# Kernel tuning notes

Measured on AMD Instinct MI355X. Metric: run time of the kernel, lower is better.

Reference implementation:

```python
import jax, jax.numpy as jnp
import numpy as np

# GATConv hyperparams hardcoded in InterGraphAttention: out_channels=32, heads=2
H = 2
C = 32
N_H = 50000
N_T = 50000
E = 1600000
D = 128
NEG_SLOPE = 0.2


def setup_inputs() -> dict:
    key = jax.random.key(0)
    ks = jax.random.split(key, 9)
    h_x = jax.random.normal(ks[0], (N_H, D), dtype=jnp.float32)
    t_x = jax.random.normal(ks[1], (N_T, D), dtype=jnp.float32)
    src = jax.random.randint(ks[2], (E,), 0, N_H)
    dst = jax.random.randint(ks[3], (E,), 0, N_T)
    # PyG's add_self_loops path first removes existing self-loops; generate edges without any
    dst = jnp.where(dst == src, (dst + 1) % N_T, dst)
    edge_index = jnp.stack([src, dst]).astype(jnp.int64)
    glorot = 1.0 / np.sqrt(D)
    W_src = jax.random.normal(ks[4], (D, H * C), dtype=jnp.float32) * glorot
    W_dst = jax.random.normal(ks[5], (D, H * C), dtype=jnp.float32) * glorot
    att_src = jax.random.normal(ks[6], (H, C), dtype=jnp.float32) * (1.0 / np.sqrt(C))
    att_dst = jax.random.normal(ks[7], (H, C), dtype=jnp.float32) * (1.0 / np.sqrt(C))
    bias = jnp.zeros((H * C,), dtype=jnp.float32)
    return {"h_x": h_x, "t_x": t_x, "edge_index": edge_index,
            "W_src": W_src, "W_dst": W_dst,
            "att_src": att_src, "att_dst": att_dst, "bias": bias}


def _gat(x_src, x_dst, src, dst, W_s, W_d, a_src, a_dst, bias):
    Ns, Nd = x_src.shape[0], x_dst.shape[0]
    xs = (x_src @ W_s).reshape(Ns, H, C)   # [Ns,H,C]
    xd = (x_dst @ W_d).reshape(Nd, H, C)   # [Nd,H,C]
    al_s = jnp.einsum('nhc,hc->nh', xs, a_src)  # [Ns,H]
    al_d = jnp.einsum('nhc,hc->nh', xd, a_dst)  # [Nd,H]
    # PyG GATConv default add_self_loops=True: append i->i for i < min(Ns,Nd)
    loop = jnp.arange(min(Ns, Nd), dtype=src.dtype)
    src2 = jnp.concatenate([src, loop])
    dst2 = jnp.concatenate([dst, loop])
    alpha = jax.nn.leaky_relu(al_s[src2] + al_d[dst2], NEG_SLOPE)  # [E2,H]
    # edge-softmax over destination neighborhoods (PyG softmax: +1e-16 in denom)
    m = jax.ops.segment_max(alpha, dst2, num_segments=Nd)
    e = jnp.exp(alpha - m[dst2])
    s = jax.ops.segment_sum(e, dst2, num_segments=Nd)
    w = e / (s[dst2] + 1e-16)                                      # [E2,H]
    msg = w[:, :, None] * xs[src2]                                 # [E2,H,C]
    out = jax.ops.segment_sum(msg, dst2, num_segments=Nd)          # [Nd,H,C]
    return out.reshape(Nd, H * C) + bias


def reference(h_x, t_x, edge_index, W_src, W_dst, att_src, att_dst, bias):
    h_in = jax.nn.elu(h_x)
    t_in = jax.nn.elu(t_x)
    src, dst = edge_index[0], edge_index[1]
    t_rep = _gat(h_in, t_in, src, dst, W_src, W_dst, att_src, att_dst, bias)
    h_rep = _gat(t_in, h_in, dst, src, W_src, W_dst, att_src, att_dst, bias)
    return (h_rep, t_rep)
```

## Files before the change

kernel.cpp:

```cpp
#include <hip/hip_runtime.h>
#include <hip/hip_bf16.h>
#include <math.h>

#define HC 64
#define DD 128
#define BSH 7
#define BW  128
#define KMAX 512
#define CHUNK 4096
#define CAP 8192
#define CAPB 6144

typedef __attribute__((ext_vector_type(8))) short bf16x8;
typedef __attribute__((ext_vector_type(4))) float f32x4;

__device__ __forceinline__ unsigned short f2bf(float f) {
  unsigned u = __float_as_uint(f);
  return (unsigned short)((u + 0x7fffu + ((u >> 16) & 1u)) >> 16);
}

__global__ __launch_bounds__(128) void build_bt(
    const float* __restrict__ Wsrc, const float* __restrict__ Wdst,
    const float* __restrict__ att_src, const float* __restrict__ att_dst,
    unsigned short* __restrict__ Bt)
{
  int j = blockIdx.x;
  int k = threadIdx.x;
  const float LOG2E = 1.44269504f;
  float v = 0.f;
  if (j < 64) {
    v = Wsrc[k * HC + j];
  } else if (j < 68) {
    int hh = j - 64;
    const float* W = (hh < 2) ? Wsrc : Wdst;
    const float* a = (hh < 2) ? att_src : att_dst;
    int h = hh & 1;
    float s = 0.f;
    for (int c = 0; c < 32; ++c)
      s = fmaf(W[k * HC + h * 32 + c], a[h * 32 + c], s);
    v = s * LOG2E;
  }
  Bt[j * DD + k] = f2bf(v);
}

__global__ __launch_bounds__(256) void node_mfma(
    const float* __restrict__ xH, const float* __restrict__ xT,
    const unsigned short* __restrict__ Bt,
    __hip_bfloat16* __restrict__ xsH, __hip_bfloat16* __restrict__ xsT,
    float* __restrict__ lsH, float* __restrict__ ldH,
    float* __restrict__ lsT, float* __restrict__ ldT,
    int NH, int NT, int blocksH)
{
  const float* x; __hip_bfloat16* xs; float* logit_s; float* logit_d; int N, blk;
  if ((int)blockIdx.x < blocksH) { x = xH; xs = xsH; logit_s = lsH; logit_d = ldH; N = NH; blk = blockIdx.x; }
  else { x = xT; xs = xsT; logit_s = lsT; logit_d = ldT; N = NT; blk = blockIdx.x - blocksH; }

  int tid  = threadIdx.x;
  int wid  = tid >> 6;
  int lane = tid & 63;
  int m    = lane & 15;
  int kg   = lane >> 4;
  int nbase = (blk * 4 + wid) * 16;
  if (nbase >= N) return;
  int nrow = nbase + m;
  int nclamp = (nrow < N) ? nrow : (N - 1);

  bf16x8 ahi[4], alo[4];
  const float* xrow = x + (size_t)nclamp * DD + kg * 8;
  #pragma unroll
  for (int kt = 0; kt < 4; ++kt) {
    float4 v0 = *(const float4*)(xrow + kt * 32);
    float4 v1 = *(const float4*)(xrow + kt * 32 + 4);
    float vv[8] = {v0.x, v0.y, v0.z, v0.w, v1.x, v1.y, v1.z, v1.w};
    #pragma unroll
    for (int i = 0; i < 8; ++i) {
      float v = vv[i];
      v = (v > 0.f) ? v : (exp2f(v * 1.44269504f) - 1.f);
      unsigned hb = __float_as_uint(v) & 0xffff0000u;
      ahi[kt][i] = (short)(hb >> 16);
      alo[kt][i] = (short)f2bf(v - __uint_as_float(hb));
    }
  }

  f32x4 acc[5];
  #pragma unroll
  for (int ct = 0; ct < 5; ++ct) acc[ct] = (f32x4){0.f, 0.f, 0.f, 0.f};
  const unsigned short* bbase = Bt + m * DD + kg * 8;
  #pragma unroll
  for (int ct = 0; ct < 5; ++ct) {
    #pragma unroll
    for (int kt = 0; kt < 4; ++kt) {
      bf16x8 b = *(const bf16x8*)(bbase + ct * 16 * DD + kt * 32);
      acc[ct] = __builtin_amdgcn_mfma_f32_16x16x32_bf16(ahi[kt], b, acc[ct], 0, 0, 0);
      acc[ct] = __builtin_amdgcn_mfma_f32_16x16x32_bf16(alo[kt], b, acc[ct], 0, 0, 0);
    }
  }

  int r0 = kg * 4;
  unsigned short* xsu = (unsigned short*)xs;
  #pragma unroll
  for (int ct = 0; ct < 4; ++ct) {
    #pragma unroll
    for (int r = 0; r < 4; ++r) {
      int n = nbase + r0 + r;
      if (n < N) xsu[(size_t)n * HC + ct * 16 + m] = f2bf(acc[ct][r]);
    }
  }
  if (m < 4) {
    float* dst = (m < 2) ? logit_s : logit_d;
    int h = m & 1;
    #pragma unroll
    for (int r = 0; r < 4; ++r) {
      int n = nbase + r0 + r;
      if (n < N) dst[n * 2 + h] = acc[4][r];
    }
  }
}

__global__ __launch_bounds__(256) void partition_atomic(
    const int* __restrict__ src, const int* __restrict__ dst, int E, int NL,
    int* __restrict__ gcurA, int* __restrict__ gcurB,
    unsigned int* __restrict__ partA, unsigned int* __restrict__ partB,
    int KA, int KB)
{
  __shared__ unsigned int stage[CHUNK];
  __shared__ int lcnt[KMAX];
  __shared__ int lbase[KMAX];
  __shared__ int lcur[KMAX];
  __shared__ int gbase[KMAX];
  int tid = threadIdx.x, bid = blockIdx.x;
  int pass = blockIdx.y;
  const int K = pass ? KB : KA;
  int* gcur = pass ? gcurB : gcurA;
  unsigned int* out = pass ? partB : partA;

  int base = bid * CHUNK;
  int E2 = E + NL;
  int lim = base + CHUNK < E2 ? base + CHUNK : E2;
  int cnt = lim - base;

  for (int i = tid; i < K; i += 256) lcnt[i] = 0;
  __syncthreads();
  for (int i = base + tid; i < lim; i += 256) {
    int s, d;
    if (i < E) { s = src[i]; d = dst[i]; } else { s = d = i - E; }
    int key = pass ? s : d;
    atomicAdd(&lcnt[key >> BSH], 1);
  }
  __syncthreads();
  if (tid < 64) {
    int carry = 0;
    for (int c0 = 0; c0 < K; c0 += 64) {
      int c = c0 + tid;
      int v = (c < K) ? lcnt[c] : 0;
      int inc = v;
      #pragma unroll
      for (int o = 1; o < 64; o <<= 1) {
        int u = __shfl_up(inc, o, 64);
        if (tid >= o) inc += u;
      }
      if (c < K) lbase[c] = inc - v + carry;
      carry += __shfl(inc, 63, 64);
    }
  }
  __syncthreads();
  for (int k = tid; k < K; k += 256) {
    lcur[k] = lbase[k];
    gbase[k] = atomicAdd(&gcur[k], lcnt[k]);
  }
  __syncthreads();
  for (int i = base + tid; i < lim; i += 256) {
    int s, d;
    if (i < E) { s = src[i]; d = dst[i]; } else { s = d = i - E; }
    int key = pass ? s : d;
    int val = pass ? d : s;
    int pos = atomicAdd(&lcur[key >> BSH], 1);
    stage[pos] = (unsigned int)val | ((unsigned int)key << 16);
  }
  __syncthreads();
  for (int i = tid; i < cnt; i += 256) {
    unsigned int wv = stage[i];
    int k = wv >> (16 + BSH);
    out[(size_t)k * CAPB + gbase[k] + (i - lbase[k])] = wv;
  }
}

__global__ __launch_bounds__(1024) void scan_offsets(
    const int* __restrict__ gcurA, const int* __restrict__ gcurB,
    int KA, int KB, int E2,
    int* __restrict__ offA, int* __restrict__ offB)
{
  __shared__ int buf[1024];
  int t = threadIdx.x;
  int v = (t < KA) ? gcurA[t] : 0;
  buf[t] = v; __syncthreads();
  #pragma unroll
  for (int off = 1; off < 1024; off <<= 1) {
    int u = (t >= off) ? buf[t - off] : 0;
    __syncthreads(); buf[t] += u; __syncthreads();
  }
  if (t < KA) offA[t] = buf[t] - v;
  if (t == 0) offA[KA] = E2;
  __syncthreads();
  int v2 = (t < KB) ? gcurB[t] : 0;
  buf[t] = v2; __syncthreads();
  #pragma unroll
  for (int off = 1; off < 1024; off <<= 1) {
    int u = (t >= off) ? buf[t - off] : 0;
    __syncthreads(); buf[t] += u; __syncthreads();
  }
  if (t < KB) offB[t] = buf[t] - v2;
  if (t == 0) offB[KB] = E2;
}

__global__ __launch_bounds__(256) void bucket_csr3(
    const unsigned int* __restrict__ partA, const int* __restrict__ cntA,
    const int* __restrict__ offA, int KA, int NA,
    const unsigned int* __restrict__ partB, const int* __restrict__ cntB,
    const int* __restrict__ offB, int KB, int NB,
    int E2, int* __restrict__ csrA, int* __restrict__ rowA,
    int* __restrict__ csrB, int* __restrict__ rowB)
{
  __shared__ int sbuf[CAP];
  __shared__ int hist[BW + 1];
  __shared__ int cur[BW];
  const unsigned int* part; const int* off; const int* cntp;
  int* csr; int* row; int k, K, N;
  if ((int)blockIdx.x < KA) { k = blockIdx.x; part = partA; off = offA; cntp = cntA; csr = csrA; row = rowA; K = KA; N = NA; }
  else { k = blockIdx.x - KA; part = partB; off = offB; cntp = cntB; csr = csrB; row = rowB; K = KB; N = NB; }
  int tid = threadIdx.x;
  int beg = off[k];
  int cnt = cntp[k];
  size_t kbase = (size_t)k * CAPB;
  int d0 = k << BSH;
  int width = (BW < N - d0) ? BW : (N - d0);

  for (int i = tid; i <= BW; i += 256) hist[i] = 0;
  __syncthreads();
  for (int i = tid; i < cnt; i += 256)
    atomicAdd(&hist[(part[kbase + i] >> 16) & (BW - 1)], 1);
  __syncthreads();
  if (tid == 0) {
    int run = 0;
    for (int j = 0; j < width; ++j) { int c = hist[j]; hist[j] = run; run += c; }
    hist[width] = run;
  }
  __syncthreads();
  if (tid < width) { cur[tid] = hist[tid]; row[d0 + tid] = beg + hist[tid]; }
  if (k == K - 1 && tid == 0) row[N] = E2;
  __syncthreads();
  if (cnt <= CAP) {
    for (int i = tid; i < cnt; i += 256) {
      unsigned int wv = part[kbase + i];
      int pos = atomicAdd(&cur[(wv >> 16) & (BW - 1)], 1);
      sbuf[pos] = wv & 0xFFFF;
    }
    __syncthreads();
    for (int i = tid; i < cnt; i += 256) csr[beg + i] = sbuf[i];
  } else {
    for (int i = tid; i < cnt; i += 256) {
      unsigned int wv = part[kbase + i];
      int pos = atomicAdd(&cur[(wv >> 16) & (BW - 1)], 1);
      csr[beg + pos] = wv & 0xFFFF;
    }
  }
}

__device__ __forceinline__ float lrelu_clamp(float a) {
  a = (a > 0.f) ? a : 0.2f * a;
  return fminf(a, 43.f);
}

__global__ __launch_bounds__(256) void csr_message5(
    const int* __restrict__ rowA, const int* __restrict__ csrA,
    const float* __restrict__ lsA, const float* __restrict__ ldA,
    const __hip_bfloat16* __restrict__ xsA, float* __restrict__ outA, int NdA,
    const int* __restrict__ rowB, const int* __restrict__ csrB,
    const float* __restrict__ lsB, const float* __restrict__ ldB,
    const __hip_bfloat16* __restrict__ xsB, float* __restrict__ outB, int NdB,
    const float* __restrict__ bias, int blocksA)
{
  const int* row; const int* csr_src; const float* logit_s; const float* logit_d;
  const __hip_bfloat16* xs; float* out; int Nd, blk;
  if ((int)blockIdx.x < blocksA) { row = rowA; csr_src = csrA; logit_s = lsA; logit_d = ldA; xs = xsA; out = outA; Nd = NdA; blk = blockIdx.x; }
  else { row = rowB; csr_src = csrB; logit_s = lsB; logit_d = ldB; xs = xsB; out = outB; Nd = NdB; blk = blockIdx.x - blocksA; }

  __shared__ int lds[4 * 232];
  int tid  = threadIdx.x;
  int wid  = tid >> 6;
  int lane = tid & 63;
  int l31  = lane & 31;
  int half = lane >> 5;
  int head = l31 >> 4;

  int* L = &lds[wid * 232];
  float* Lf = (float*)L;
  int sv_w = (half ? 40 : 0) + l31;
  int w0_w = (half ? 160 : 80) + l31;
  int w1_w = (half ? 200 : 120) + l31;
  const int4*   svq = (const int4*)  (L  + (half ? 40 : 0));
  const float4* wq  = (const float4*)(Lf + (half ? (head ? 200 : 160)
                                                 : (head ? 120 : 80)));
  const unsigned* xs2 = (const unsigned*)xs;
  const float2* ls2 = (const float2*)logit_s;

  int d = blk * 8 + (wid << 1) + half;
  int beg = 0, end = 0;
  float2 ld2 = {0.f, 0.f};
  if (d < Nd) {
    beg = row[d]; end = row[d + 1];
    ld2 = ((const float2*)logit_d)[d];
  }

  int nt = ((end - beg) + 31) >> 5;
  nt = max(nt, __shfl_xor(nt, 32, 64));

  float2 accA = {0.f, 0.f}, accB = {0.f, 0.f};
  float s0 = 0.f, s1 = 0.f;
  int myPos = beg;

#define STEP(SV, W, ACC) {                                         \
    unsigned xv = xs2[(SV) * 32 + l31];                            \
    ACC.x = fmaf((W), __uint_as_float(xv << 16), ACC.x);           \
    ACC.y = fmaf((W), __uint_as_float(xv & 0xffff0000u), ACC.y);   \
  }

  for (int tile = 0; tile < nt; ++tile, myPos += 32) {
    int tc = end - myPos; tc = tc < 0 ? 0 : (tc > 32 ? 32 : tc);
    int sv = 0; float e0 = 0.f, e1 = 0.f;
    if (l31 < tc) {
      sv = csr_src[myPos + l31];
      float2 l2 = ls2[sv];
      e0 = exp2f(lrelu_clamp(l2.x + ld2.x));
      e1 = exp2f(lrelu_clamp(l2.y + ld2.y));
    }
    s0 += e0; s1 += e1;
    L[sv_w]       = sv;
    Lf[w0_w]      = e0;
    Lf[w1_w]      = e1;
    asm volatile("s_waitcnt lgkmcnt(0)" ::: "memory");
    int tcmax = max(tc, __shfl_xor(tc, 32, 64));
    int nq = (tcmax + 3) >> 2;
    for (int q = 0; q < nq; ++q) {
      int4   s4 = svq[q];
      float4 w4 = wq[q];
      STEP(s4.x, w4.x, accA)
      STEP(s4.y, w4.y, accB)
      STEP(s4.z, w4.z, accA)
      STEP(s4.w, w4.w, accB)
    }
  }
#undef STEP

  #pragma unroll
  for (int off = 16; off > 0; off >>= 1) {
    s0 += __shfl_xor(s0, off, 64);
    s1 += __shfl_xor(s1, off, 64);
  }
  float sD = (l31 & 16) ? s1 : s0;
  float inv = 1.f / (sD + 1e-16f);

  if (d < Nd) {
    float2 b2 = ((const float2*)bias)[l31];
    float2 o;
    o.x = (accA.x + accB.x) * inv + b2.x;
    o.y = (accA.y + accB.y) * inv + b2.y;
    ((float2*)out)[(size_t)d * 32 + l31] = o;
  }
}

extern "C" void kernel_launch(void* const* d_in, const int* in_sizes, int n_in,
                              void* d_out, int out_size, void* d_ws, size_t ws_size,
                              hipStream_t stream)
{
  const float* h_x   = (const float*)d_in[0];
  const float* t_x   = (const float*)d_in[1];
  const int*   edge  = (const int*)d_in[2];
  const float* W_src = (const float*)d_in[3];
  const float* W_dst = (const float*)d_in[4];
  const float* att_s = (const float*)d_in[5];
  const float* att_d = (const float*)d_in[6];
  const float* bias  = (const float*)d_in[7];

  int NH = in_sizes[0] / DD;
  int NT = in_sizes[1] / DD;
  int E  = in_sizes[2] / 2;
  int NL = (NH < NT) ? NH : NT;
  int E2 = E + NL;
  const int* srcA = edge;
  const int* dstA = edge + E;

  int KA = (NT + BW - 1) >> BSH;
  int KB = (NH + BW - 1) >> BSH;
  int B  = (E2 + CHUNK - 1) / CHUNK;

  char* w = (char*)d_ws;
  size_t used = 0;
  auto alloc = [&](size_t bytes) {
    char* p = w + used; used = (used + bytes + 255) & ~(size_t)255; return p;
  };
  __hip_bfloat16* xsA = (__hip_bfloat16*)alloc((size_t)NH * HC * 2);
  __hip_bfloat16* xsB = (__hip_bfloat16*)alloc((size_t)NT * HC * 2);
  float* lsA  = (float*)alloc((size_t)NH * 2 * 4);
  float* ldB  = (float*)alloc((size_t)NH * 2 * 4);
  float* lsB  = (float*)alloc((size_t)NT * 2 * 4);
  float* ldA  = (float*)alloc((size_t)NT * 2 * 4);
  int* gcur   = (int*)alloc((size_t)(KA + KB) * 4);
  int* gcurA  = gcur;
  int* gcurB  = gcur + KA;
  int* offA   = (int*)alloc((size_t)(KA + 1) * 4);
  int* offB   = (int*)alloc((size_t)(KB + 1) * 4);
  int* rowT   = (int*)alloc((size_t)(NT + 1) * 4);
  int* rowH   = (int*)alloc((size_t)(NH + 1) * 4);
  unsigned int* partA = (unsigned int*)alloc((size_t)KA * CAPB * 4);
  unsigned int* partB = (unsigned int*)alloc((size_t)KB * CAPB * 4);
  int* csrT   = (int*)alloc((size_t)E2 * 4);
  int* csrH   = (int*)alloc((size_t)E2 * 4);
  unsigned short* Bt = (unsigned short*)alloc((size_t)80 * DD * 2);

  float* out   = (float*)d_out;
  float* out_h = out;
  float* out_t = out + (size_t)NH * HC;

  build_bt<<<80, 128, 0, stream>>>(W_src, W_dst, att_s, att_d, Bt);

  int bH = (NH + 63) / 64, bT = (NT + 63) / 64;
  node_mfma<<<bH + bT, 256, 0, stream>>>(
      h_x, t_x, Bt, xsA, xsB, lsA, ldB, lsB, ldA, NH, NT, bH);

  hipMemsetAsync(gcur, 0, (size_t)(KA + KB) * 4, stream);
  partition_atomic<<<dim3(B, 2), 256, 0, stream>>>(
      srcA, dstA, E, NL, gcurA, gcurB, partA, partB, KA, KB);
  scan_offsets<<<1, 1024, 0, stream>>>(gcurA, gcurB, KA, KB, E2, offA, offB);
  bucket_csr3<<<KA + KB, 256, 0, stream>>>(
      partA, gcurA, offA, KA, NT, partB, gcurB, offB, KB, NH,
      E2, csrT, rowT, csrH, rowH);

  int gA = (NT + 7) / 8, gB = (NH + 7) / 8;
  csr_message5<<<gA + gB, 256, 0, stream>>>(
      rowT, csrT, lsA, ldA, xsA, out_t, NT,
      rowH, csrH, lsB, ldB, xsB, out_h, NH, bias, gA);
}
```

Baseline: 235.7 us.

## Fuse node projection with edge partition and drop memset and scan kernels

```diff
diff --git a/kernel.cpp b/kernel.cpp
--- a/kernel.cpp
+++ b/kernel.cpp
@@ -22,7 +22,7 @@
 __global__ __launch_bounds__(128) void build_bt(
     const float* __restrict__ Wsrc, const float* __restrict__ Wdst,
     const float* __restrict__ att_src, const float* __restrict__ att_dst,
-    unsigned short* __restrict__ Bt)
+    unsigned short* __restrict__ Bt, int* __restrict__ gcur, int KK)
 {
   int j = blockIdx.x;
   int k = threadIdx.x;
@@ -41,195 +41,190 @@
     v = s * LOG2E;
   }
   Bt[j * DD + k] = f2bf(v);
-}
-
-__global__ __launch_bounds__(256) void node_mfma(
+  if (j == 0) {
+    for (int i = k; i < KK; i += 128) gcur[i] = 0;
+  }
+}
+
+__global__ __launch_bounds__(512) void fused_front(
     const float* __restrict__ xH, const float* __restrict__ xT,
     const unsigned short* __restrict__ Bt,
     __hip_bfloat16* __restrict__ xsH, __hip_bfloat16* __restrict__ xsT,
     float* __restrict__ lsH, float* __restrict__ ldH,
     float* __restrict__ lsT, float* __restrict__ ldT,
-    int NH, int NT, int blocksH)
-{
-  const float* x; __hip_bfloat16* xs; float* logit_s; float* logit_d; int N, blk;
-  if ((int)blockIdx.x < blocksH) { x = xH; xs = xsH; logit_s = lsH; logit_d = ldH; N = NH; blk = blockIdx.x; }
-  else { x = xT; xs = xsT; logit_s = lsT; logit_d = ldT; N = NT; blk = blockIdx.x - blocksH; }
-
-  int tid  = threadIdx.x;
-  int wid  = tid >> 6;
-  int lane = tid & 63;
-  int m    = lane & 15;
-  int kg   = lane >> 4;
-  int nbase = (blk * 4 + wid) * 16;
-  if (nbase >= N) return;
-  int nrow = nbase + m;
-  int nclamp = (nrow < N) ? nrow : (N - 1);
-
-  bf16x8 ahi[4], alo[4];
-  const float* xrow = x + (size_t)nclamp * DD + kg * 8;
-  #pragma unroll
-  for (int kt = 0; kt < 4; ++kt) {
-    float4 v0 = *(const float4*)(xrow + kt * 32);
-    float4 v1 = *(const float4*)(xrow + kt * 32 + 4);
-    float vv[8] = {v0.x, v0.y, v0.z, v0.w, v1.x, v1.y, v1.z, v1.w};
-    #pragma unroll
-    for (int i = 0; i < 8; ++i) {
-      float v = vv[i];
-      v = (v > 0.f) ? v : (exp2f(v * 1.44269504f) - 1.f);
-      unsigned hb = __float_as_uint(v) & 0xffff0000u;
-      ahi[kt][i] = (short)(hb >> 16);
-      alo[kt][i] = (short)f2bf(v - __uint_as_float(hb));
-    }
-  }
-
-  f32x4 acc[5];
-  #pragma unroll
-  for (int ct = 0; ct < 5; ++ct) acc[ct] = (f32x4){0.f, 0.f, 0.f, 0.f};
-  const unsigned short* bbase = Bt + m * DD + kg * 8;
-  #pragma unroll
-  for (int ct = 0; ct < 5; ++ct) {
-    #pragma unroll
-    for (int kt = 0; kt < 4; ++kt) {
-      bf16x8 b = *(const bf16x8*)(bbase + ct * 16 * DD + kt * 32);
-      acc[ct] = __builtin_amdgcn_mfma_f32_16x16x32_bf16(ahi[kt], b, acc[ct], 0, 0, 0);
-      acc[ct] = __builtin_amdgcn_mfma_f32_16x16x32_bf16(alo[kt], b, acc[ct], 0, 0, 0);
-    }
-  }
-
-  int r0 = kg * 4;
-  unsigned short* xsu = (unsigned short*)xs;
-  #pragma unroll
-  for (int ct = 0; ct < 4; ++ct) {
-    #pragma unroll
-    for (int r = 0; r < 4; ++r) {
-      int n = nbase + r0 + r;
-      if (n < N) xsu[(size_t)n * HC + ct * 16 + m] = f2bf(acc[ct][r]);
-    }
-  }
-  if (m < 4) {
-    float* dst = (m < 2) ? logit_s : logit_d;
-    int h = m & 1;
-    #pragma unroll
-    for (int r = 0; r < 4; ++r) {
-      int n = nbase + r0 + r;
-      if (n < N) dst[n * 2 + h] = acc[4][r];
-    }
-  }
-}
-
-__global__ __launch_bounds__(256) void partition_atomic(
+    int NH, int NT, int blocksH, int nodeB,
     const int* __restrict__ src, const int* __restrict__ dst, int E, int NL,
     int* __restrict__ gcurA, int* __restrict__ gcurB,
     unsigned int* __restrict__ partA, unsigned int* __restrict__ partB,
     int KA, int KB)
 {
+  __shared__ unsigned int raw[CHUNK];
   __shared__ unsigned int stage[CHUNK];
   __shared__ int lcnt[KMAX];
   __shared__ int lbase[KMAX];
   __shared__ int lcur[KMAX];
   __shared__ int gbase[KMAX];
-  int tid = threadIdx.x, bid = blockIdx.x;
-  int pass = blockIdx.y;
-  const int K = pass ? KB : KA;
-  int* gcur = pass ? gcurB : gcurA;
-  unsigned int* out = pass ? partB : partA;
-
+
+  int tid = threadIdx.x;
+
+  if ((int)blockIdx.x < nodeB) {
+    const float* x; __hip_bfloat16* xs; float* logit_s; float* logit_d; int N, blk;
+    if ((int)blockIdx.x < blocksH) { x = xH; xs = xsH; logit_s = lsH; logit_d = ldH; N = NH; blk = blockIdx.x; }
+    else { x = xT; xs = xsT; logit_s = lsT; logit_d = ldT; N = NT; blk = blockIdx.x - blocksH; }
+
+    int wid  = tid >> 6;
+    int lane = tid & 63;
+    int m    = lane & 15;
+    int kg   = lane >> 4;
+    int nbase = (blk * 8 + wid) * 16;
+    if (nbase >= N) return;
+    int nrow = nbase + m;
+    int nclamp = (nrow < N) ? nrow : (N - 1);
+
+    bf16x8 ahi[4], alo[4];
+    const float* xrow = x + (size_t)nclamp * DD + kg * 8;
+    #pragma unroll
+    for (int kt = 0; kt < 4; ++kt) {
+      float4 v0 = *(const float4*)(xrow + kt * 32);
+      float4 v1 = *(const float4*)(xrow + kt * 32 + 4);
+      float vv[8] = {v0.x, v0.y, v0.z, v0.w, v1.x, v1.y, v1.z, v1.w};
+      #pragma unroll
+      for (int i = 0; i < 8; ++i) {
+        float v = vv[i];
+        v = (v > 0.f) ? v : (exp2f(v * 1.44269504f) - 1.f);
+        unsigned hb = __float_as_uint(v) & 0xffff0000u;
+        ahi[kt][i] = (short)(hb >> 16);
+        alo[kt][i] = (short)f2bf(v - __uint_as_float(hb));
+      }
+    }
+
+    f32x4 acc[5];
+    #pragma unroll
+    for (int ct = 0; ct < 5; ++ct) acc[ct] = (f32x4){0.f, 0.f, 0.f, 0.f};
+    const unsigned short* bbase = Bt + m * DD + kg * 8;
+    #pragma unroll
+    for (int ct = 0; ct < 5; ++ct) {
+      #pragma unroll
+      for (int kt = 0; kt < 4; ++kt) {
+        bf16x8 b = *(const bf16x8*)(bbase + ct * 16 * DD + kt * 32);
+        acc[ct] = __builtin_amdgcn_mfma_f32_16x16x32_bf16(ahi[kt], b, acc[ct], 0, 0, 0);
+        acc[ct] = __builtin_amdgcn_mfma_f32_16x16x32_bf16(alo[kt], b, acc[ct], 0, 0, 0);
+      }
+    }
+
+    int r0 = kg * 4;
+    unsigned short* xsu = (unsigned short*)xs;
+    #pragma unroll
+    for (int ct = 0; ct < 4; ++ct) {
+      #pragma unroll
+      for (int r = 0; r < 4; ++r) {
+        int n = nbase + r0 + r;
+        if (n < N) xsu[(size_t)n * HC + ct * 16 + m] = f2bf(acc[ct][r]);
+      }
+    }
+    if (m < 4) {
+      float* dstp = (m < 2) ? logit_s : logit_d;
+      int h = m & 1;
+      #pragma unroll
+      for (int r = 0; r < 4; ++r) {
+        int n = nbase + r0 + r;
+        if (n < N) dstp[n * 2 + h] = acc[4][r];
+      }
+    }
+    return;
+  }
+
+  int bid = blockIdx.x - nodeB;
   int base = bid * CHUNK;
   int E2 = E + NL;
   int lim = base + CHUNK < E2 ? base + CHUNK : E2;
   int cnt = lim - base;
 
-  for (int i = tid; i < K; i += 256) lcnt[i] = 0;
+  for (int i = base + tid; i < lim; i += 512) {
+    unsigned s, d;
+    if (i < E) { s = (unsigned)src[i]; d = (unsigned)dst[i]; }
+    else       { s = d = (unsigned)(i - E); }
+    raw[i - base] = s | (d << 16);
+  }
   __syncthreads();
-  for (int i = base + tid; i < lim; i += 256) {
-    int s, d;
-    if (i < E) { s = src[i]; d = dst[i]; } else { s = d = i - E; }
-    int key = pass ? s : d;
-    atomicAdd(&lcnt[key >> BSH], 1);
-  }
-  __syncthreads();
-  if (tid < 64) {
-    int carry = 0;
-    for (int c0 = 0; c0 < K; c0 += 64) {
-      int c = c0 + tid;
-      int v = (c < K) ? lcnt[c] : 0;
-      int inc = v;
-      #pragma unroll
-      for (int o = 1; o < 64; o <<= 1) {
-        int u = __shfl_up(inc, o, 64);
-        if (tid >= o) inc += u;
+
+  for (int p = 0; p < 2; ++p) {
+    const int K = p ? KB : KA;
+    int* gcur = p ? gcurB : gcurA;
+    unsigned int* outp = p ? partB : partA;
+
+    for (int k2 = tid; k2 < K; k2 += 512) lcnt[k2] = 0;
+    __syncthreads();
+    for (int i = tid; i < cnt; i += 512) {
+      unsigned w = raw[i];
+      unsigned key = p ? (w & 0xffffu) : (w >> 16);
+      atomicAdd(&lcnt[key >> BSH], 1);
+    }
+    __syncthreads();
+    if (tid < 64) {
+      int carry = 0;
+      for (int c0 = 0; c0 < K; c0 += 64) {
+        int c = c0 + tid;
+        int v = (c < K) ? lcnt[c] : 0;
+        int inc = v;
+        #pragma unroll
+        for (int o = 1; o < 64; o <<= 1) {
+          int u = __shfl_up(inc, o, 64);
+          if (tid >= o) inc += u;
+        }
+        if (c < K) lbase[c] = inc - v + carry;
+        carry += __shfl(inc, 63, 64);
       }
-      if (c < K) lbase[c] = inc - v + carry;
-      carry += __shfl(inc, 63, 64);
-    }
-  }
-  __syncthreads();
-  for (int k = tid; k < K; k += 256) {
-    lcur[k] = lbase[k];
-    gbase[k] = atomicAdd(&gcur[k], lcnt[k]);
-  }
-  __syncthreads();
-  for (int i = base + tid; i < lim; i += 256) {
-    int s, d;
-    if (i < E) { s = src[i]; d = dst[i]; } else { s = d = i - E; }
-    int key = pass ? s : d;
-    int val = pass ? d : s;
-    int pos = atomicAdd(&lcur[key >> BSH], 1);
-    stage[pos] = (unsigned int)val | ((unsigned int)key << 16);
-  }
-  __syncthreads();
-  for (int i = tid; i < cnt; i += 256) {
-    unsigned int wv = stage[i];
-    int k = wv >> (16 + BSH);
-    out[(size_t)k * CAPB + gbase[k] + (i - lbase[k])] = wv;
-  }
-}
-
-__global__ __launch_bounds__(1024) void scan_offsets(
-    const int* __restrict__ gcurA, const int* __restrict__ gcurB,
-    int KA, int KB, int E2,
-    int* __restrict__ offA, int* __restrict__ offB)
-{
-  __shared__ int buf[1024];
-  int t = threadIdx.x;
-  int v = (t < KA) ? gcurA[t] : 0;
-  buf[t] = v; __syncthreads();
-  #pragma unroll
-  for (int off = 1; off < 1024; off <<= 1) {
-    int u = (t >= off) ? buf[t - off] : 0;
-    __syncthreads(); buf[t] += u; __syncthreads();
-  }
-  if (t < KA) offA[t] = buf[t] - v;
-  if (t == 0) offA[KA] = E2;
-  __syncthreads();
-  int v2 = (t < KB) ? gcurB[t] : 0;
-  buf[t] = v2; __syncthreads();
-  #pragma unroll
-  for (int off = 1; off < 1024; off <<= 1) {
-    int u = (t >= off) ? buf[t - off] : 0;
-    __syncthreads(); buf[t] += u; __syncthreads();
-  }
-  if (t < KB) offB[t] = buf[t] - v2;
-  if (t == 0) offB[KB] = E2;
-}
-
-__global__ __launch_bounds__(256) void bucket_csr3(
+    }
+    __syncthreads();
+    for (int k2 = tid; k2 < K; k2 += 512) {
+      lcur[k2] = lbase[k2];
+      gbase[k2] = atomicAdd(&gcur[k2], lcnt[k2]);
+    }
+    __syncthreads();
+    for (int i = tid; i < cnt; i += 512) {
+      unsigned w = raw[i];
+      unsigned key = p ? (w & 0xffffu) : (w >> 16);
+      unsigned val = p ? (w >> 16) : (w & 0xffffu);
+      int pos = atomicAdd(&lcur[key >> BSH], 1);
+      stage[pos] = val | (key << 16);
+    }
+    __syncthreads();
+    for (int i = tid; i < cnt; i += 512) {
+      unsigned wv = stage[i];
+      int kk = wv >> (16 + BSH);
+      outp[(size_t)kk * CAPB + gbase[kk] + (i - lbase[kk])] = wv;
+    }
+    __syncthreads();
+  }
+}
+
+__global__ __launch_bounds__(256) void bucket_csr4(
     const unsigned int* __restrict__ partA, const int* __restrict__ cntA,
-    const int* __restrict__ offA, int KA, int NA,
+    int KA, int NA,
     const unsigned int* __restrict__ partB, const int* __restrict__ cntB,
-    const int* __restrict__ offB, int KB, int NB,
+    int KB, int NB,
     int E2, int* __restrict__ csrA, int* __restrict__ rowA,
     int* __restrict__ csrB, int* __restrict__ rowB)
 {
   __shared__ int sbuf[CAP];
   __shared__ int hist[BW + 1];
   __shared__ int cur[BW];
-  const unsigned int* part; const int* off; const int* cntp;
+  __shared__ int red[256];
+  const unsigned int* part; const int* cntp;
   int* csr; int* row; int k, K, N;
-  if ((int)blockIdx.x < KA) { k = blockIdx.x; part = partA; off = offA; cntp = cntA; csr = csrA; row = rowA; K = KA; N = NA; }
-  else { k = blockIdx.x - KA; part = partB; off = offB; cntp = cntB; csr = csrB; row = rowB; K = KB; N = NB; }
+  if ((int)blockIdx.x < KA) { k = blockIdx.x; part = partA; cntp = cntA; csr = csrA; row = rowA; K = KA; N = NA; }
+  else { k = blockIdx.x - KA; part = partB; cntp = cntB; csr = csrB; row = rowB; K = KB; N = NB; }
   int tid = threadIdx.x;
-  int beg = off[k];
+
+  int psum = 0;
+  for (int j = tid; j < k; j += 256) psum += cntp[j];
+  red[tid] = psum; __syncthreads();
+  for (int s = 128; s > 0; s >>= 1) {
+    if (tid < s) red[tid] += red[tid + s];
+    __syncthreads();
+  }
+  int beg = red[0];
   int cnt = cntp[k];
   size_t kbase = (size_t)k * CAPB;
   int d0 = k << BSH;
@@ -408,8 +403,6 @@
   int* gcur   = (int*)alloc((size_t)(KA + KB) * 4);
   int* gcurA  = gcur;
   int* gcurB  = gcur + KA;
-  int* offA   = (int*)alloc((size_t)(KA + 1) * 4);
-  int* offB   = (int*)alloc((size_t)(KB + 1) * 4);
   int* rowT   = (int*)alloc((size_t)(NT + 1) * 4);
   int* rowH   = (int*)alloc((size_t)(NH + 1) * 4);
   unsigned int* partA = (unsigned int*)alloc((size_t)KA * CAPB * 4);
@@ -422,18 +415,17 @@
   float* out_h = out;
   float* out_t = out + (size_t)NH * HC;
 
-  build_bt<<<80, 128, 0, stream>>>(W_src, W_dst, att_s, att_d, Bt);
-
-  int bH = (NH + 63) / 64, bT = (NT + 63) / 64;
-  node_mfma<<<bH + bT, 256, 0, stream>>>(
-      h_x, t_x, Bt, xsA, xsB, lsA, ldB, lsB, ldA, NH, NT, bH);
-
-  hipMemsetAsync(gcur, 0, (size_t)(KA + KB) * 4, stream);
-  partition_atomic<<<dim3(B, 2), 256, 0, stream>>>(
+  build_bt<<<80, 128, 0, stream>>>(W_src, W_dst, att_s, att_d, Bt,
+                                   gcur, KA + KB);
+
+  int bH = (NH + 127) / 128, bT = (NT + 127) / 128;
+  int nodeB = bH + bT;
+  fused_front<<<nodeB + B, 512, 0, stream>>>(
+      h_x, t_x, Bt, xsA, xsB, lsA, ldB, lsB, ldA, NH, NT, bH, nodeB,
       srcA, dstA, E, NL, gcurA, gcurB, partA, partB, KA, KB);
-  scan_offsets<<<1, 1024, 0, stream>>>(gcurA, gcurB, KA, KB, E2, offA, offB);
-  bucket_csr3<<<KA + KB, 256, 0, stream>>>(
-      partA, gcurA, offA, KA, NT, partB, gcurB, offB, KB, NH,
+
+  bucket_csr4<<<KA + KB, 256, 0, stream>>>(
+      partA, gcurA, KA, NT, partB, gcurB, KB, NH,
       E2, csrT, rowT, csrH, rowH);
 
   int gA = (NT + 7) / 8, gB = (NH + 7) / 8;
```

Measured after the change: 221.3 us. 1.07x faster.
